# Optimization experiments

Hardware: AMD Instinct MI355X
Metric: run time of the kernel (lower is better)

## Reference

```python
import jax, jax.numpy as jnp
import numpy as np

RESO = 64
PAD = 0.1
SCALE = 8.0
PLANES = {'xz': (0, 2), 'xy': (0, 1), 'yz': (1, 2)}
PLANE_ORDER = ['xz', 'xy', 'yz']


def normalize_coordinate(p, plane):
    i, j = PLANES[plane]
    xy = jnp.stack([p[..., i], p[..., j]], axis=-1)
    xy = xy / (1.0 + PAD + 1e-3) + 0.5
    return jnp.clip(xy, 0.0, 1.0 - 1e-5)


def coordinate2index(xy, reso):
    x = (xy * reso).astype(jnp.int32)
    return x[..., 0] + reso * x[..., 1]  # (B, T)


def resblock(x, W0, b0, W1, b1, Ws):
    # ResnetBlockFC: fc_1(relu(fc_0(relu(x)))) + shortcut(x)
    net = jnp.maximum(x, 0.0) @ W0 + b0
    dx = jnp.maximum(net, 0.0) @ W1 + b1
    return x @ Ws + dx


def scatter_max_pool(c, idx_flat, num_seg):
    # c: (B, T, h); idx_flat: (B*T,) batch-offset plane indices
    B, T, h = c.shape
    pooled = jax.ops.segment_max(c.reshape(B * T, h), idx_flat, num_segments=num_seg)
    return pooled[idx_flat].reshape(B, T, h)


def plane_feature(p, c, plane):
    # scatter_mean of c into (B, c_dim, RESO, RESO); empty cells -> 0
    B, T, cd = c.shape
    R2 = RESO * RESO
    idx = coordinate2index(normalize_coordinate(p / SCALE, plane), RESO)
    idxf = (idx + jnp.arange(B, dtype=jnp.int32)[:, None] * R2).reshape(-1)
    sums = jax.ops.segment_sum(c.reshape(B * T, cd), idxf, num_segments=B * R2)
    cnt = jax.ops.segment_sum(jnp.ones((B * T,), c.dtype), idxf, num_segments=B * R2)
    mean = sums / jnp.maximum(cnt, 1.0)[:, None]
    return mean.reshape(B, R2, cd).transpose(0, 2, 1).reshape(B, cd, RESO, RESO)


def forward(p, fc_pos_W, fc_pos_b, blocks_W0, blocks_b0, blocks_W1, blocks_b1, blocks_Ws, fc_c_W, fc_c_b):
    B, T, _ = p.shape
    R2 = RESO * RESO
    offs = jnp.arange(B, dtype=jnp.int32)[:, None] * R2
    idx = {k: (coordinate2index(normalize_coordinate(p / SCALE, k), RESO) + offs).reshape(-1)
           for k in PLANE_ORDER}

    net = p @ fc_pos_W + fc_pos_b  # (B, T, 3h)
    net = resblock(net, blocks_W0[0], blocks_b0[0], blocks_W1[0], blocks_b1[0], blocks_Ws[0])
    n_blocks = blocks_W0.shape[0]
    for i in range(1, n_blocks):
        pooled = sum(scatter_max_pool(net, idx[k], B * R2) for k in PLANE_ORDER)
        meanp = jnp.broadcast_to(net.mean(axis=1, keepdims=True), net.shape)
        net = jnp.concatenate([net, pooled, meanp], axis=-1)  # (B, T, 3h)
        net = resblock(net, blocks_W0[i], blocks_b0[i], blocks_W1[i], blocks_b1[i], blocks_Ws[i])

    c = net @ fc_c_W + fc_c_b  # (B, T, c_dim)
    fea = jnp.stack([plane_feature(p, c, k) for k in PLANE_ORDER], axis=0)
    return fea  # (3, B, c_dim, RESO, RESO) in order xz, xy, yz


def setup_inputs() -> dict:
    key = jax.random.key(0)
    ks = jax.random.split(key, 10)
    B, T, dim = 16, 8192, 3
    h, c_dim, nb = 128, 128, 5
    s = 0.05
    return {
        'p': jax.random.normal(ks[0], (B, T, dim), jnp.float32) * 2.0,
        'fc_pos_W': jax.random.normal(ks[1], (dim, 3 * h), jnp.float32) * s,
        'fc_pos_b': jnp.zeros((3 * h,), jnp.float32),
        'blocks_W0': jax.random.normal(ks[2], (nb, 3 * h, h), jnp.float32) * s,
        'blocks_b0': jnp.zeros((nb, h), jnp.float32),
        'blocks_W1': jax.random.normal(ks[3], (nb, h, h), jnp.float32) * s,
        'blocks_b1': jnp.zeros((nb, h), jnp.float32),
        'blocks_Ws': jax.random.normal(ks[4], (nb, 3 * h, h), jnp.float32) * s,
        'fc_c_W': jax.random.normal(ks[5], (h, c_dim), jnp.float32) * s,
        'fc_c_b': jnp.zeros((c_dim,), jnp.float32),
    }


def reference(p, fc_pos_W, fc_pos_b, blocks_W0, blocks_b0, blocks_W1, blocks_b1, blocks_Ws, fc_c_W, fc_c_b):
    return forward(p, fc_pos_W, fc_pos_b, blocks_W0, blocks_b0, blocks_W1, blocks_b1, blocks_Ws, fc_c_W, fc_c_b)
```

## Files before the change

kernel.cpp:

```cpp
#include <hip/hip_runtime.h>

#define BT (16 * 8192)
#define NB 5
#define NCELL 65536
typedef unsigned int uint;
typedef unsigned short ushort;
typedef __attribute__((ext_vector_type(8))) _Float16 half8;
typedef __attribute__((ext_vector_type(2))) __fp16 fp16x2;
typedef __attribute__((ext_vector_type(2))) _Float16 half2v;
typedef __attribute__((ext_vector_type(4))) float f32x4;


__device__ __forceinline__ uint f2h2(float a, float b) {
    fp16x2 h = __builtin_amdgcn_cvt_pkrtz(a, b);
    return *(uint*)&h;
}
__device__ __forceinline__ float h2f_lo(uint u) { half2v h = *(half2v*)&u; return (float)h[0]; }
__device__ __forceinline__ float h2f_hi(uint u) { half2v h = *(half2v*)&u; return (float)h[1]; }
__device__ __forceinline__ uint pk_add(uint a, uint b) {
    uint d; asm("v_pk_add_f16 %0, %1, %2" : "=v"(d) : "v"(a), "v"(b)); return d;
}
__device__ __forceinline__ uint pk_max(uint a, uint b) {
    uint d; asm("v_pk_max_f16 %0, %1, %2" : "=v"(d) : "v"(a), "v"(b)); return d;
}

__device__ __forceinline__ uint relu2(uint u) {
    uint m = (u >> 15) & 0x00010001u;
    return u & ~(m * 0xffffu);
}
__device__ __forceinline__ half8 relu8(half8 a) {
    uint4 u = *(uint4*)&a;
    u.x = relu2(u.x); u.y = relu2(u.y); u.z = relu2(u.z); u.w = relu2(u.w);
    return *(half8*)&u;
}
__device__ __forceinline__ f32x4 bcast4(float x) { return (f32x4){x, x, x, x}; }
__device__ __forceinline__ f32x4 mfma16(half8 a, half8 b, f32x4 c) {
    return __builtin_amdgcn_mfma_f32_16x16x32_f16(a, b, c, 0, 0, 0);
}

__global__ void k_idx(const float* __restrict__ p, int* __restrict__ idx,
                      int4* __restrict__ idx4) {
    int r = blockIdx.x * 256 + threadIdx.x;
    if (r >= BT) return;
    float p0 = p[3 * r + 0], p1 = p[3 * r + 1], p2 = p[3 * r + 2];
    const float DEN = (float)(1.0 + 0.1 + 1e-3);
    const float HI  = (float)(1.0 - 1e-5);
    int b = r >> 13;
    float x0 = fminf(fmaxf((p0 / 8.0f) / DEN + 0.5f, 0.0f), HI);
    float x1 = fminf(fmaxf((p1 / 8.0f) / DEN + 0.5f, 0.0f), HI);
    float x2 = fminf(fmaxf((p2 / 8.0f) / DEN + 0.5f, 0.0f), HI);
    int i0 = (int)(x0 * 64.0f);
    int i1 = (int)(x1 * 64.0f);
    int i2 = (int)(x2 * 64.0f);
    int base = b << 12;
    int exz = base + i0 + (i2 << 6);
    int exy = base + i0 + (i1 << 6);
    int eyz = base + i1 + (i2 << 6);
    idx[r] = exz; idx[BT + r] = exy; idx[2 * BT + r] = eyz;
    idx4[r] = make_int4(exz, exy, eyz, 0);
}

__global__ void k_hist(const int* __restrict__ idx, int* __restrict__ cnt) {
    int r = blockIdx.x * 256 + threadIdx.x;
    if (r >= BT) return;
    atomicAdd(cnt + idx[r], 1);
    atomicAdd(cnt + NCELL + idx[BT + r], 1);
    atomicAdd(cnt + 2 * NCELL + idx[2 * BT + r], 1);
}

__global__ __launch_bounds__(1024) void k_scan(const int* __restrict__ cnt,
                                               int* __restrict__ starts,
                                               int* __restrict__ cursor) {
    __shared__ int sc[1024];
    int pl = blockIdx.x, t = threadIdx.x;
    const int* c = cnt + pl * NCELL;
    int base = t * 64;
    int s = 0;
    for (int i = 0; i < 64; ++i) s += c[base + i];
    sc[t] = s;
    __syncthreads();
    for (int off = 1; off < 1024; off <<= 1) {
        int v = (t >= off) ? sc[t - off] : 0;
        __syncthreads();
        sc[t] += v;
        __syncthreads();
    }
    int run = sc[t] - s;
    for (int i = 0; i < 64; ++i) {
        int cell = base + i;
        starts[pl * NCELL + cell] = run;
        cursor[pl * NCELL + cell] = run;
        run += c[cell];
    }
}

__global__ void k_scatter_order(const int* __restrict__ idx, int* __restrict__ cursor,
                                int* __restrict__ order) {
    int r = blockIdx.x * 256 + threadIdx.x;
    if (r >= BT) return;
    for (int pl = 0; pl < 3; ++pl) {
        int cell = idx[pl * BT + r];
        int pos = atomicAdd(cursor + pl * NCELL + cell, 1);
        order[pl * BT + pos] = r;
    }
}

__global__ void k_wconv(const float* __restrict__ W0, const float* __restrict__ W1,
                        const float* __restrict__ Ws, const float* __restrict__ Wc,
                        ushort* __restrict__ wb) {
    int mat = blockIdx.y;
    int K = (mat < 5 || (mat >= 10 && mat < 15)) ? 384 : 128;
    int e = blockIdx.x * 256 + threadIdx.x;
    if (e >= K * 128) return;
    const float* src;
    size_t doff;
    if (mat < 5)       { src = W0 + (size_t)mat * 49152;        doff = (size_t)mat * 49152; }
    else if (mat < 10) { src = W1 + (size_t)(mat - 5) * 16384;  doff = 245760 + (size_t)(mat - 5) * 16384; }
    else if (mat < 15) { src = Ws + (size_t)(mat - 10) * 49152; doff = 327680 + (size_t)(mat - 10) * 49152; }
    else               { src = Wc;                              doff = 573440; }
    int ko = e & 31, n = (e >> 5) & 127, kt = e >> 12;
    wb[doff + e] = (ushort)f2h2(src[(size_t)(kt * 32 + ko) * 128 + n], 0.0f);
}

__global__ __launch_bounds__(128) void k_meanvec(const float* __restrict__ meanB,
                                                 const ushort* __restrict__ wb0,
                                                 const float* __restrict__ b0v,
                                                 const ushort* __restrict__ wbs,
                                                 const float* __restrict__ b1v,
                                                 float* __restrict__ rv0,
                                                 float* __restrict__ rvS) {
    __shared__ float ms[128];
    int b = blockIdx.x, n = threadIdx.x;
    ms[n] = meanB[b * 128 + n];
    __syncthreads();
    float s0 = b0v[n], ss = b1v[n];
#pragma unroll 4
    for (int k = 0; k < 128; ++k) {
        float mv = ms[k];
        int kt = 8 + (k >> 5), ko = k & 31;
        float w0 = h2f_lo((uint)wb0[kt * 4096 + n * 32 + ko]);
        float ws = h2f_lo((uint)wbs[kt * 4096 + n * 32 + ko]);
        s0 = fmaf(fmaxf(mv, 0.0f), w0, s0);
        ss = fmaf(mv, ws, ss);
    }
    rv0[b * 128 + n] = s0;
    rvS[b * 128 + n] = ss;
}

__global__ __launch_bounds__(256) void k_segmax(const uint* __restrict__ netu,
                                                const int* __restrict__ starts,
                                                const int* __restrict__ cnt,
                                                const int* __restrict__ order,
                                                uint* __restrict__ segu) {
    int g = blockIdx.x * 4 + (threadIdx.x >> 6);
    int l = threadIdx.x & 63;
    int n = cnt[g];
    if (n == 0) return;
    int pl = g >> 16;
    const int* ord = order + pl * BT + starts[g];
    uint m = 0xFC00FC00u;
    int i = 0;
    for (; i + 4 <= n; i += 4) {
        uint a = netu[(size_t)ord[i] * 64 + l];
        uint b = netu[(size_t)ord[i + 1] * 64 + l];
        uint c = netu[(size_t)ord[i + 2] * 64 + l];
        uint d = netu[(size_t)ord[i + 3] * 64 + l];
        m = pk_max(m, pk_max(pk_max(a, b), pk_max(c, d)));
    }
    int rem = n - i;
    if (rem > 0) {
        uint a = netu[(size_t)ord[i] * 64 + l];
        uint b = (rem > 1) ? netu[(size_t)ord[i + 1] * 64 + l] : a;
        uint c = (rem > 2) ? netu[(size_t)ord[i + 2] * 64 + l] : a;
        m = pk_max(m, pk_max(a, pk_max(b, c)));
    }
    segu[(size_t)g * 64 + l] = m;
}

template <int MODE>
__global__ __launch_bounds__(512, 6) void k_resblock(
    const float* __restrict__ p, const uint* __restrict__ netu,
    const int4* __restrict__ idx4, const ushort* __restrict__ seg,
    const float* __restrict__ rv0, const float* __restrict__ rvS,
    const float* __restrict__ Wp, const float* __restrict__ bp,
    const ushort* __restrict__ wb0, const float* __restrict__ b0v,
    const ushort* __restrict__ wb1, const float* __restrict__ b1v,
    const ushort* __restrict__ wbs,
    ushort* __restrict__ out, float* __restrict__ meanW) {
    constexpr int LDA = (MODE == 0) ? 392 : 264;
    constexpr int NKT = (MODE == 0) ? 12 : 8;
    __shared__ __align__(16) ushort aT[64 * LDA];
    __shared__ __align__(16) ushort hT[64 * 136];
    const int t = threadIdx.x;
    const int rowBase = blockIdx.x * 64;
    const int bb = rowBase >> 13;

    if constexpr (MODE == 0) {
        for (int f = t; f < 3072; f += 512) {
            int row = f / 48, g = f - row * 48;
            const float* pr = p + (size_t)(rowBase + row) * 3;
            float p0 = pr[0], p1 = pr[1], p2 = pr[2];
            int k0 = g * 8;
            uint d[4];
#pragma unroll
            for (int w = 0; w < 4; ++w) {
                int k = k0 + 2 * w;
                float v0 = bp[k]     + p0 * Wp[k]     + p1 * Wp[384 + k]     + p2 * Wp[768 + k];
                float v1 = bp[k + 1] + p0 * Wp[k + 1] + p1 * Wp[384 + k + 1] + p2 * Wp[768 + k + 1];
                d[w] = f2h2(v0, v1);
            }
            *(uint4*)(aT + row * LDA + k0) = make_uint4(d[0], d[1], d[2], d[3]);
        }
    } else {
        const uint4* nsrc = (const uint4*)netu;
#pragma unroll
        for (int i = 0; i < 2; ++i) {
            int f = t + 512 * i;
            int row = f >> 4, cu = f & 15;
            *(uint4*)(aT + row * LDA + cu * 8) = nsrc[(size_t)(rowBase + row) * 16 + cu];
        }
#pragma unroll
        for (int i = 0; i < 2; ++i) {
            int f = t + 512 * i;
            int row = f >> 4, grp = f & 15;
            int4 cc = idx4[rowBase + row];
            const uint4* s0 = (const uint4*)(seg + ((size_t)cc.x) * 128 + grp * 8);
            const uint4* s1 = (const uint4*)(seg + ((size_t)NCELL + cc.y) * 128 + grp * 8);
            const uint4* s2 = (const uint4*)(seg + ((size_t)2 * NCELL + cc.z) * 128 + grp * 8);
            uint4 A = *s0, B = *s1, C = *s2;
            uint4 d;
            d.x = pk_add(pk_add(A.x, B.x), C.x);
            d.y = pk_add(pk_add(A.y, B.y), C.y);
            d.z = pk_add(pk_add(A.z, B.z), C.z);
            d.w = pk_add(pk_add(A.w, B.w), C.w);
            *(uint4*)(aT + row * LDA + 128 + grp * 8) = d;
        }
    }
    __syncthreads();

    const int l = t & 63, wid = t >> 6;
    const int n0 = wid * 16;
    const int lm = l & 15, lg = l >> 4;
    const ushort* w0 = wb0 + n0 * 32;
    const ushort* w1 = wb1 + n0 * 32;
    const ushort* ws = wbs + n0 * 32;

    f32x4 acc0[4], accS[4];
    {
        float bi, si;
        if constexpr (MODE == 0) { bi = b0v[n0 + lm];            si = b1v[n0 + lm]; }
        else                     { bi = rv0[bb * 128 + n0 + lm]; si = rvS[bb * 128 + n0 + lm]; }
#pragma unroll
        for (int im = 0; im < 4; ++im) { acc0[im] = bcast4(bi); accS[im] = bcast4(si); }
    }
#pragma unroll
    for (int kt = 0; kt < NKT; ++kt) {
        half8 b0 = *(const half8*)(w0 + kt * 4096 + lm * 32 + lg * 8);
        half8 bs = *(const half8*)(ws + kt * 4096 + lm * 32 + lg * 8);
#pragma unroll
        for (int im = 0; im < 4; ++im) {
            half8 a = *(const half8*)(aT + (im * 16 + lm) * LDA + kt * 32 + lg * 8);
            acc0[im] = mfma16(relu8(a), b0, acc0[im]);
            accS[im] = mfma16(a, bs, accS[im]);
        }
    }
#pragma unroll
    for (int im = 0; im < 4; ++im)
#pragma unroll
        for (int j = 0; j < 4; ++j) {
            int row = im * 16 + lg * 4 + j;
            hT[row * 136 + n0 + lm] = (ushort)f2h2(fmaxf(acc0[im][j], 0.0f), 0.0f);
        }
    __syncthreads();

#pragma unroll
    for (int kt = 0; kt < 4; ++kt) {
        half8 b = *(const half8*)(w1 + kt * 4096 + lm * 32 + lg * 8);
#pragma unroll
        for (int im = 0; im < 4; ++im) {
            half8 a = *(const half8*)(hT + (im * 16 + lm) * 136 + kt * 32 + lg * 8);
            accS[im] = mfma16(a, b, accS[im]);
        }
    }

#pragma unroll
    for (int im = 0; im < 4; ++im)
#pragma unroll
        for (int j = 0; j < 4; ++j) {
            int row = rowBase + im * 16 + lg * 4 + j;
            out[(size_t)row * 128 + n0 + lm] = (ushort)f2h2(accS[im][j], 0.0f);
        }

    if (meanW) {
        float s = 0.0f;
#pragma unroll
        for (int im = 0; im < 4; ++im)
#pragma unroll
            for (int j = 0; j < 4; ++j) s += accS[im][j];
        s += __shfl_xor(s, 16);
        s += __shfl_xor(s, 32);
        if (l < 16) atomicAdd(meanW + bb * 128 + n0 + l, s * (1.0f / 8192.0f));
    }
}

__device__ __forceinline__ void mfma_gemm3(const ushort* __restrict__ aLDS, int lda, int nk,
                                           const ushort* __restrict__ wb, int lm, int lg,
                                           f32x4 acc[4][2]) {
    for (int kt = 0; kt < nk; ++kt) {
        half8 b0 = *(const half8*)(wb + kt * 4096 + lm * 32 + lg * 8);
        half8 b1 = *(const half8*)(wb + kt * 4096 + (16 + lm) * 32 + lg * 8);
#pragma unroll
        for (int im = 0; im < 4; ++im) {
            half8 a = *(const half8*)(aLDS + (im * 16 + lm) * lda + kt * 32 + lg * 8);
            acc[im][0] = mfma16(a, b0, acc[im][0]);
            acc[im][1] = mfma16(a, b1, acc[im][1]);
        }
    }
}

__global__ __launch_bounds__(256, 2) void k_fcc(const uint* __restrict__ netu,
                                                const ushort* __restrict__ wbc,
                                                const float* __restrict__ bc,
                                                ushort* __restrict__ cout) {
    __shared__ __align__(16) ushort aT[64 * 136];
    const int t = threadIdx.x;
    const int rowBase = blockIdx.x * 64;
    const uint4* nsrc = (const uint4*)netu;
#pragma unroll
    for (int i = 0; i < 4; ++i) {
        int u = t + 256 * i;
        int row = u >> 4, cu = u & 15;
        *(uint4*)(aT + row * 136 + cu * 8) = nsrc[(size_t)(rowBase + row) * 16 + cu];
    }
    __syncthreads();
    const int l = t & 63, wid = t >> 6;
    const int n0 = wid * 32;
    const int lm = l & 15, lg = l >> 4;
    f32x4 acc[4][2];
    {
        float ci0 = bc[n0 + lm], ci1 = bc[n0 + 16 + lm];
#pragma unroll
        for (int im = 0; im < 4; ++im) { acc[im][0] = bcast4(ci0); acc[im][1] = bcast4(ci1); }
    }
    mfma_gemm3(aT, 136, 4, wbc + n0 * 32, lm, lg, acc);
#pragma unroll
    for (int im = 0; im < 4; ++im)
#pragma unroll
        for (int ic = 0; ic < 2; ++ic)
#pragma unroll
            for (int j = 0; j < 4; ++j) {
                int row = rowBase + im * 16 + lg * 4 + j;
                int col = n0 + ic * 16 + lm;
                cout[(size_t)row * 128 + col] = (ushort)f2h2(acc[im][ic][j], 0.0f);
            }
}

__global__ __launch_bounds__(256) void k_segsum(const uint* __restrict__ cp,
                                                const int* __restrict__ starts,
                                                const int* __restrict__ cnt,
                                                const int* __restrict__ order,
                                                float* __restrict__ sums, int pl) {
    int cell = blockIdx.x * 4 + (threadIdx.x >> 6);
    int l = threadIdx.x & 63;
    int n = cnt[pl * NCELL + cell];
    if (n == 0) return;
    const int* ord = order + pl * BT + starts[pl * NCELL + cell];
    float s0 = 0.f, s1 = 0.f;
    int i = 0;
    for (; i + 4 <= n; i += 4) {
        uint a = cp[(size_t)ord[i] * 64 + l];
        uint b = cp[(size_t)ord[i + 1] * 64 + l];
        uint c = cp[(size_t)ord[i + 2] * 64 + l];
        uint d = cp[(size_t)ord[i + 3] * 64 + l];
        s0 += (h2f_lo(a) + h2f_lo(b)) + (h2f_lo(c) + h2f_lo(d));
        s1 += (h2f_hi(a) + h2f_hi(b)) + (h2f_hi(c) + h2f_hi(d));
    }
    int rem = n - i;
    if (rem > 0) {
        uint a = cp[(size_t)ord[i] * 64 + l];
        uint b = (rem > 1) ? cp[(size_t)ord[i + 1] * 64 + l] : 0u;
        uint c = (rem > 2) ? cp[(size_t)ord[i + 2] * 64 + l] : 0u;
        s0 += h2f_lo(a) + (h2f_lo(b) + h2f_lo(c));
        s1 += h2f_hi(a) + (h2f_hi(b) + h2f_hi(c));
    }
    *(float2*)(sums + (size_t)cell * 128 + 2 * l) = make_float2(s0, s1);
}

__global__ __launch_bounds__(256) void k_fin(const float* __restrict__ sums,
                                             const int* __restrict__ cnt,
                                             float* __restrict__ out, int pl) {
    __shared__ float tile[32][33];
    int t = threadIdx.x;
    int tx = t & 31, ty = t >> 5;
    int cl0 = (blockIdx.x & 127) << 5;
    int ch0 = (blockIdx.x >> 7) << 5;
    int b = blockIdx.y;
    int bc = b << 12;
#pragma unroll
    for (int j = 0; j < 4; ++j)
        tile[ty + 8 * j][tx] = sums[(size_t)(bc + cl0 + ty + 8 * j) * 128 + ch0 + tx];
    __syncthreads();
#pragma unroll
    for (int j = 0; j < 4; ++j) {
        int ch = ch0 + ty + 8 * j;
        int cl = cl0 + tx;
        int cn = cnt[pl * NCELL + bc + cl];
        float v = cn > 0 ? tile[tx][ty + 8 * j] / (float)cn : 0.0f;
        out[((size_t)((pl * 16 + b) * 128 + ch) << 12) + cl] = v;
    }
}

extern "C" void kernel_launch(void* const* d_in, const int* in_sizes, int n_in,
                              void* d_out, int out_size, void* d_ws, size_t ws_size,
                              hipStream_t stream) {
    const float* p  = (const float*)d_in[0];
    const float* Wp = (const float*)d_in[1];
    const float* bp = (const float*)d_in[2];
    const float* W0 = (const float*)d_in[3];
    const float* b0 = (const float*)d_in[4];
    const float* W1 = (const float*)d_in[5];
    const float* b1 = (const float*)d_in[6];
    const float* Ws = (const float*)d_in[7];
    const float* Wc = (const float*)d_in[8];
    const float* bc = (const float*)d_in[9];
    float* out = (float*)d_out;

    ushort* net    = (ushort*)d_ws;
    ushort* seg    = net + 16777216;
    float*  sums   = (float*)seg;
    ushort* wb     = seg + 25165824;
    int*    idx    = (int*)(wb + 589824);
    int*    order  = idx + 393216;
    int*    cnt    = order + 393216;
    int*    starts = cnt + 196608;
    int*    cursor = starts + 196608;
    float*  meanB  = (float*)(cursor + 196608);
    float*  rv0    = meanB + 2 * 2048;
    float*  rvS    = rv0 + 2048;
    int4*   idx4   = (int4*)(rvS + 2048);

    k_idx<<<512, 256, 0, stream>>>(p, idx, idx4);
    (void)hipMemsetAsync(cnt, 0, 3 * NCELL * 4, stream);
    k_hist<<<512, 256, 0, stream>>>(idx, cnt);
    k_scan<<<3, 1024, 0, stream>>>(cnt, starts, cursor);
    k_scatter_order<<<512, 256, 0, stream>>>(idx, cursor, order);
    k_wconv<<<dim3(192, 16), 256, 0, stream>>>(W0, W1, Ws, Wc, wb);

    (void)hipMemsetAsync(meanB, 0, 2048 * 4, stream);
    k_resblock<0><<<2048, 512, 0, stream>>>(
        p, nullptr, nullptr, nullptr, nullptr, nullptr, Wp, bp,
        wb, b0, wb + 245760, b1, wb + 327680, net, meanB);

    for (int i = 1; i < NB; ++i) {
        const ushort* wb0i = wb + (size_t)i * 49152;
        const ushort* wb1i = wb + 245760 + (size_t)i * 16384;
        const ushort* wbsi = wb + 327680 + (size_t)i * 49152;
        k_segmax<<<49152, 256, 0, stream>>>((const uint*)net, starts, cnt, order, (uint*)seg);
        k_meanvec<<<16, 128, 0, stream>>>(meanB + ((i - 1) & 1) * 2048,
                                          wb0i, b0 + i * 128, wbsi, b1 + i * 128, rv0, rvS);
        float* mw = nullptr;
        if (i < NB - 1) {
            mw = meanB + (i & 1) * 2048;
            (void)hipMemsetAsync(mw, 0, 2048 * 4, stream);
        }
        k_resblock<1><<<2048, 512, 0, stream>>>(
            nullptr, (const uint*)net, idx4, seg, rv0, rvS, nullptr, nullptr,
            wb0i, nullptr, wb1i, nullptr, wbsi, net, mw);
    }

    k_fcc<<<2048, 256, 0, stream>>>((const uint*)net, wb + 573440, bc, net);

    for (int pl = 0; pl < 3; ++pl) {
        k_segsum<<<16384, 256, 0, stream>>>((const uint*)net, starts, cnt, order, sums, pl);
        k_fin<<<dim3(512, 16), 256, 0, stream>>>(sums, cnt, out, pl);
    }
}
```

Measured before the change: 767.8 us.

## Fuse mean-vector into segmax, fuse segsum with finalize, alias resblock smem

Folds the per-batch mean-vector GEMV into extra blocks of the segmax launch. The three per-plane segment-sum and transpose/finalize pairs become a single kernel that accumulates 64 cells into shared memory and writes normalized output directly, which removes the fp32 sums round trip through global memory. meanB now gets four buffers zeroed once, so the per-iteration memsets go away. The resblock hidden tile reuses the input tile's shared memory behind an added barrier, which lets the occupancy hint rise to 8 waves per SIMD for MODE 1; the extra barrier and register pressure are the trade-offs.

Measured after the change: 756.2 us. No clear change (-1.5%).

```diff
diff --git a/kernel.cpp b/kernel.cpp
--- a/kernel.cpp
+++ b/kernel.cpp
@@ -122,38 +122,42 @@
     wb[doff + e] = (ushort)f2h2(src[(size_t)(kt * 32 + ko) * 128 + n], 0.0f);
 }
 
-__global__ __launch_bounds__(128) void k_meanvec(const float* __restrict__ meanB,
-                                                 const ushort* __restrict__ wb0,
-                                                 const float* __restrict__ b0v,
-                                                 const ushort* __restrict__ wbs,
-                                                 const float* __restrict__ b1v,
-                                                 float* __restrict__ rv0,
-                                                 float* __restrict__ rvS) {
-    __shared__ float ms[128];
-    int b = blockIdx.x, n = threadIdx.x;
-    ms[n] = meanB[b * 128 + n];
-    __syncthreads();
-    float s0 = b0v[n], ss = b1v[n];
-#pragma unroll 4
-    for (int k = 0; k < 128; ++k) {
-        float mv = ms[k];
-        int kt = 8 + (k >> 5), ko = k & 31;
-        float w0 = h2f_lo((uint)wb0[kt * 4096 + n * 32 + ko]);
-        float ws = h2f_lo((uint)wbs[kt * 4096 + n * 32 + ko]);
-        s0 = fmaf(fmaxf(mv, 0.0f), w0, s0);
-        ss = fmaf(mv, ws, ss);
-    }
-    rv0[b * 128 + n] = s0;
-    rvS[b * 128 + n] = ss;
-}
-
 __global__ __launch_bounds__(256) void k_segmax(const uint* __restrict__ netu,
                                                 const int* __restrict__ starts,
                                                 const int* __restrict__ cnt,
                                                 const int* __restrict__ order,
-                                                uint* __restrict__ segu) {
-    int g = blockIdx.x * 4 + (threadIdx.x >> 6);
-    int l = threadIdx.x & 63;
+                                                uint* __restrict__ segu,
+                                                const float* __restrict__ meanPrev,
+                                                const ushort* __restrict__ wb0,
+                                                const float* __restrict__ b0v,
+                                                const ushort* __restrict__ wbs,
+                                                const float* __restrict__ b1v,
+                                                float* __restrict__ rv0,
+                                                float* __restrict__ rvS) {
+    int t = threadIdx.x;
+    if (blockIdx.x >= 49152) {
+        __shared__ float ms[128];
+        int b = blockIdx.x - 49152;
+        if (t < 128) ms[t] = meanPrev[b * 128 + t];
+        __syncthreads();
+        if (t < 128) {
+            float s0 = b0v[t], ss = b1v[t];
+#pragma unroll 4
+            for (int k = 0; k < 128; ++k) {
+                float mv = ms[k];
+                int kt = 8 + (k >> 5), ko = k & 31;
+                float w0 = h2f_lo((uint)wb0[kt * 4096 + t * 32 + ko]);
+                float ws = h2f_lo((uint)wbs[kt * 4096 + t * 32 + ko]);
+                s0 = fmaf(fmaxf(mv, 0.0f), w0, s0);
+                ss = fmaf(mv, ws, ss);
+            }
+            rv0[b * 128 + t] = s0;
+            rvS[b * 128 + t] = ss;
+        }
+        return;
+    }
+    int g = blockIdx.x * 4 + (t >> 6);
+    int l = t & 63;
     int n = cnt[g];
     if (n == 0) return;
     int pl = g >> 16;
@@ -178,7 +182,7 @@
 }
 
 template <int MODE>
-__global__ __launch_bounds__(512, 6) void k_resblock(
+__global__ __launch_bounds__(512, MODE == 0 ? 6 : 8) void k_resblock(
     const float* __restrict__ p, const uint* __restrict__ netu,
     const int4* __restrict__ idx4, const ushort* __restrict__ seg,
     const float* __restrict__ rv0, const float* __restrict__ rvS,
@@ -190,7 +194,7 @@
     constexpr int LDA = (MODE == 0) ? 392 : 264;
     constexpr int NKT = (MODE == 0) ? 12 : 8;
     __shared__ __align__(16) ushort aT[64 * LDA];
-    __shared__ __align__(16) ushort hT[64 * 136];
+    ushort* hT = aT;
     const int t = threadIdx.x;
     const int rowBase = blockIdx.x * 64;
     const int bb = rowBase >> 13;
@@ -224,10 +228,9 @@
             int f = t + 512 * i;
             int row = f >> 4, grp = f & 15;
             int4 cc = idx4[rowBase + row];
-            const uint4* s0 = (const uint4*)(seg + ((size_t)cc.x) * 128 + grp * 8);
-            const uint4* s1 = (const uint4*)(seg + ((size_t)NCELL + cc.y) * 128 + grp * 8);
-            const uint4* s2 = (const uint4*)(seg + ((size_t)2 * NCELL + cc.z) * 128 + grp * 8);
-            uint4 A = *s0, B = *s1, C = *s2;
+            uint4 A = *(const uint4*)(seg + ((size_t)cc.x) * 128 + grp * 8);
+            uint4 B = *(const uint4*)(seg + ((size_t)NCELL + cc.y) * 128 + grp * 8);
+            uint4 C = *(const uint4*)(seg + ((size_t)2 * NCELL + cc.z) * 128 + grp * 8);
             uint4 d;
             d.x = pk_add(pk_add(A.x, B.x), C.x);
             d.y = pk_add(pk_add(A.y, B.y), C.y);
@@ -264,6 +267,8 @@
             accS[im] = mfma16(a, bs, accS[im]);
         }
     }
+    __syncthreads();
+
 #pragma unroll
     for (int im = 0; im < 4; ++im)
 #pragma unroll
@@ -355,58 +360,58 @@
             }
 }
 
-__global__ __launch_bounds__(256) void k_segsum(const uint* __restrict__ cp,
+__global__ __launch_bounds__(256) void k_segfin(const uint* __restrict__ cp,
                                                 const int* __restrict__ starts,
                                                 const int* __restrict__ cnt,
                                                 const int* __restrict__ order,
-                                                float* __restrict__ sums, int pl) {
-    int cell = blockIdx.x * 4 + (threadIdx.x >> 6);
-    int l = threadIdx.x & 63;
-    int n = cnt[pl * NCELL + cell];
-    if (n == 0) return;
-    const int* ord = order + pl * BT + starts[pl * NCELL + cell];
-    float s0 = 0.f, s1 = 0.f;
-    int i = 0;
-    for (; i + 4 <= n; i += 4) {
-        uint a = cp[(size_t)ord[i] * 64 + l];
-        uint b = cp[(size_t)ord[i + 1] * 64 + l];
-        uint c = cp[(size_t)ord[i + 2] * 64 + l];
-        uint d = cp[(size_t)ord[i + 3] * 64 + l];
-        s0 += (h2f_lo(a) + h2f_lo(b)) + (h2f_lo(c) + h2f_lo(d));
-        s1 += (h2f_hi(a) + h2f_hi(b)) + (h2f_hi(c) + h2f_hi(d));
-    }
-    int rem = n - i;
-    if (rem > 0) {
-        uint a = cp[(size_t)ord[i] * 64 + l];
-        uint b = (rem > 1) ? cp[(size_t)ord[i + 1] * 64 + l] : 0u;
-        uint c = (rem > 2) ? cp[(size_t)ord[i + 2] * 64 + l] : 0u;
-        s0 += h2f_lo(a) + (h2f_lo(b) + h2f_lo(c));
-        s1 += h2f_hi(a) + (h2f_hi(b) + h2f_hi(c));
-    }
-    *(float2*)(sums + (size_t)cell * 128 + 2 * l) = make_float2(s0, s1);
-}
-
-__global__ __launch_bounds__(256) void k_fin(const float* __restrict__ sums,
-                                             const int* __restrict__ cnt,
-                                             float* __restrict__ out, int pl) {
-    __shared__ float tile[32][33];
-    int t = threadIdx.x;
-    int tx = t & 31, ty = t >> 5;
-    int cl0 = (blockIdx.x & 127) << 5;
-    int ch0 = (blockIdx.x >> 7) << 5;
-    int b = blockIdx.y;
-    int bc = b << 12;
-#pragma unroll
-    for (int j = 0; j < 4; ++j)
-        tile[ty + 8 * j][tx] = sums[(size_t)(bc + cl0 + ty + 8 * j) * 128 + ch0 + tx];
-    __syncthreads();
-#pragma unroll
-    for (int j = 0; j < 4; ++j) {
-        int ch = ch0 + ty + 8 * j;
-        int cl = cl0 + tx;
-        int cn = cnt[pl * NCELL + bc + cl];
-        float v = cn > 0 ? tile[tx][ty + 8 * j] / (float)cn : 0.0f;
-        out[((size_t)((pl * 16 + b) * 128 + ch) << 12) + cl] = v;
+                                                float* __restrict__ out) {
+    __shared__ float tile[64 * 130];
+    const int t = threadIdx.x;
+    const int w = t >> 6, l = t & 63;
+    const int bx = blockIdx.x;
+    const int pl = bx >> 10;
+    const int rem = bx & 1023;
+    const int b = rem >> 6;
+    const int cl0 = (rem & 63) << 6;
+    const int gbase = pl * NCELL + (b << 12) + cl0;
+    const int* ordp = order + pl * BT;
+
+    for (int i = 0; i < 16; ++i) {
+        int cellLocal = w * 16 + i;
+        int g = gbase + cellLocal;
+        int n = cnt[g];
+        float s0 = 0.f, s1 = 0.f;
+        if (n > 0) {
+            const int* ord = ordp + starts[g];
+            int j = 0;
+            for (; j + 4 <= n; j += 4) {
+                uint a = cp[(size_t)ord[j] * 64 + l];
+                uint bq = cp[(size_t)ord[j + 1] * 64 + l];
+                uint c = cp[(size_t)ord[j + 2] * 64 + l];
+                uint d = cp[(size_t)ord[j + 3] * 64 + l];
+                s0 += (h2f_lo(a) + h2f_lo(bq)) + (h2f_lo(c) + h2f_lo(d));
+                s1 += (h2f_hi(a) + h2f_hi(bq)) + (h2f_hi(c) + h2f_hi(d));
+            }
+            int rm = n - j;
+            if (rm > 0) {
+                uint a = cp[(size_t)ord[j] * 64 + l];
+                uint bq = (rm > 1) ? cp[(size_t)ord[j + 1] * 64 + l] : 0u;
+                uint c = (rm > 2) ? cp[(size_t)ord[j + 2] * 64 + l] : 0u;
+                s0 += h2f_lo(a) + (h2f_lo(bq) + h2f_lo(c));
+                s1 += h2f_hi(a) + (h2f_hi(bq) + h2f_hi(c));
+            }
+        }
+        *(float2*)(tile + cellLocal * 130 + 2 * l) = make_float2(s0, s1);
+    }
+    __syncthreads();
+
+    int cn = cnt[gbase + l];
+    float inv = cn > 0 ? 1.0f / (float)cn : 0.0f;
+    size_t obase = (((size_t)((pl * 16 + b) * 128)) << 12) + cl0 + l;
+#pragma unroll 8
+    for (int j = 0; j < 32; ++j) {
+        int ch = w * 32 + j;
+        out[obase + ((size_t)ch << 12)] = tile[l * 130 + ch] * inv;
     }
 }
 
@@ -427,7 +432,6 @@
 
     ushort* net    = (ushort*)d_ws;
     ushort* seg    = net + 16777216;
-    float*  sums   = (float*)seg;
     ushort* wb     = seg + 25165824;
     int*    idx    = (int*)(wb + 589824);
     int*    order  = idx + 393216;
@@ -435,7 +439,7 @@
     int*    starts = cnt + 196608;
     int*    cursor = starts + 196608;
     float*  meanB  = (float*)(cursor + 196608);
-    float*  rv0    = meanB + 2 * 2048;
+    float*  rv0    = meanB + 4 * 2048;
     float*  rvS    = rv0 + 2048;
     int4*   idx4   = (int4*)(rvS + 2048);
 
@@ -445,8 +449,8 @@
     k_scan<<<3, 1024, 0, stream>>>(cnt, starts, cursor);
     k_scatter_order<<<512, 256, 0, stream>>>(idx, cursor, order);
     k_wconv<<<dim3(192, 16), 256, 0, stream>>>(W0, W1, Ws, Wc, wb);
-
-    (void)hipMemsetAsync(meanB, 0, 2048 * 4, stream);
+    (void)hipMemsetAsync(meanB, 0, 4 * 2048 * 4, stream);
+
     k_resblock<0><<<2048, 512, 0, stream>>>(
         p, nullptr, nullptr, nullptr, nullptr, nullptr, Wp, bp,
         wb, b0, wb + 245760, b1, wb + 327680, net, meanB);
@@ -455,14 +459,10 @@
         const ushort* wb0i = wb + (size_t)i * 49152;
         const ushort* wb1i = wb + 245760 + (size_t)i * 16384;
         const ushort* wbsi = wb + 327680 + (size_t)i * 49152;
-        k_segmax<<<49152, 256, 0, stream>>>((const uint*)net, starts, cnt, order, (uint*)seg);
-        k_meanvec<<<16, 128, 0, stream>>>(meanB + ((i - 1) & 1) * 2048,
-                                          wb0i, b0 + i * 128, wbsi, b1 + i * 128, rv0, rvS);
-        float* mw = nullptr;
-        if (i < NB - 1) {
-            mw = meanB + (i & 1) * 2048;
-            (void)hipMemsetAsync(mw, 0, 2048 * 4, stream);
-        }
+        k_segmax<<<49168, 256, 0, stream>>>((const uint*)net, starts, cnt, order, (uint*)seg,
+                                            meanB + (i - 1) * 2048, wb0i, b0 + i * 128,
+                                            wbsi, b1 + i * 128, rv0, rvS);
+        float* mw = (i < NB - 1) ? meanB + i * 2048 : nullptr;
         k_resblock<1><<<2048, 512, 0, stream>>>(
             nullptr, (const uint*)net, idx4, seg, rv0, rvS, nullptr, nullptr,
             wb0i, nullptr, wb1i, nullptr, wbsi, net, mw);
@@ -470,8 +470,5 @@
 
     k_fcc<<<2048, 256, 0, stream>>>((const uint*)net, wb + 573440, bc, net);
 
-    for (int pl = 0; pl < 3; ++pl) {
-        k_segsum<<<16384, 256, 0, stream>>>((const uint*)net, starts, cnt, order, sums, pl);
-        k_fin<<<dim3(512, 16), 256, 0, stream>>>(sums, cnt, out, pl);
-    }
-}
+    k_segfin<<<3072, 256, 0, stream>>>((const uint*)net, starts, cnt, order, out);
+}
```
